# Performance work log

Measured on AMD Instinct MI355X. Metric: run time of the kernel, lower is better.

Reference implementation:

```python
import jax, jax.numpy as jnp
import numpy as np

N = 65536      # total nodes (cells) in batch
E = 262144     # edges per edge type
T = 3          # edge types: row, col, diag
D = 128        # hidden_dim
HG = 4         # gat_heads
DHG = D // HG  # 32, GAT head dim
HH = 4         # hgt_heads
DHH = D // HH  # 32, HGT head dim
B = 32         # boards per batch
SLOPE = 0.2
EPS = 1e-6


def setup_inputs():
    ks = jax.random.split(jax.random.key(0), 32)
    def nrm(i, shape, s=0.05):
        return (jax.random.normal(ks[i], shape) * s).astype(jnp.float32)
    inp = {
        'x_cell': nrm(0, (N, D), 1.0),
        'z_h': nrm(1, (B, D), 1.0),
        'x_cell_embedded': nrm(2, (N, D), 1.0),
        'edge_index': jax.random.randint(ks[3], (T, 2, E), 0, N, dtype=jnp.int32),
        'batch_size': B,
        # GAT conv 1 (one GATConv per edge type, summed)
        'gat1_W': nrm(4, (T, D, D), 0.09),
        'gat1_asrc': nrm(5, (T, HG, DHG), 0.12),
        'gat1_adst': nrm(6, (T, HG, DHG), 0.12),
        'gat1_b': jnp.zeros((T, D), jnp.float32),
        # GAT conv 2
        'gat2_W': nrm(7, (T, D, D), 0.09),
        'gat2_asrc': nrm(8, (T, HG, DHG), 0.12),
        'gat2_adst': nrm(9, (T, HG, DHG), 0.12),
        'gat2_b': jnp.zeros((T, D), jnp.float32),
        # RMSNorms
        'norm1_s': jnp.ones((D,), jnp.float32),
        'norm2_s': jnp.ones((D,), jnp.float32),
        'norm3_s': jnp.ones((D,), jnp.float32),
        # HGT (single node type 'cell', T edge types)
        'hgt_Wk': nrm(10, (D, D), 0.09), 'hgt_bk': jnp.zeros((D,), jnp.float32),
        'hgt_Wq': nrm(11, (D, D), 0.09), 'hgt_bq': jnp.zeros((D,), jnp.float32),
        'hgt_Wv': nrm(12, (D, D), 0.09), 'hgt_bv': jnp.zeros((D,), jnp.float32),
        'hgt_arel': nrm(13, (T, HH, DHH, DHH), 0.15),
        'hgt_mrel': nrm(14, (T, HH, DHH, DHH), 0.15),
        'hgt_prel': jnp.ones((T, HH), jnp.float32),
        'hgt_Wo': nrm(15, (D, D), 0.09), 'hgt_bo': jnp.zeros((D,), jnp.float32),
        'hgt_skip': jnp.ones((), jnp.float32),
        # input injection
        'inj_W': nrm(16, (D, D), 0.09), 'inj_b': jnp.zeros((D,), jnp.float32),
        # FiLM
        'film_W1': nrm(17, (D, 2 * D), 0.09), 'film_b1': jnp.zeros((2 * D,), jnp.float32),
        'film_W2': nrm(18, (2 * D, 2 * D), 0.001), 'film_b2': jnp.zeros((2 * D,), jnp.float32),
    }
    return inp


def _rmsnorm(x, scale):
    return scale * x * jax.lax.rsqrt(jnp.mean(x * x, axis=-1, keepdims=True) + EPS)


def _res(x_old, x_new, scale):
    return jax.nn.leaky_relu(x_old + _rmsnorm(x_new, scale), SLOPE)


def _gat_sum(x, W, asrc, adst, b, src, dst):
    """HeteroConv(sum) over T GATConvs (concat heads, add_self_loops)."""
    loop = jnp.arange(N, dtype=src.dtype)
    def one(Wt, a_s, a_d, bt, s, t):
        s = jnp.concatenate([s, loop])   # self loops
        t = jnp.concatenate([t, loop])
        h = (x @ Wt).reshape(N, HG, DHG)             # [N,H,Dh]
        alpha_src = (h * a_s).sum(-1)                # [N,H]
        alpha_dst = (h * a_d).sum(-1)
        e = jax.nn.leaky_relu(alpha_src[s] + alpha_dst[t], SLOPE)  # [E+N,H]
        m = jax.ops.segment_max(e, t, num_segments=N)
        ex = jnp.exp(e - m[t])
        denom = jax.ops.segment_sum(ex, t, num_segments=N)
        alpha = ex / (denom[t] + 1e-16)
        out = jax.ops.segment_sum(alpha[:, :, None] * h[s], t, num_segments=N)
        return out.reshape(N, D) + bt
    return jax.vmap(one)(W, asrc, adst, b, src, dst).sum(0)


def _hgt(x, Wk, bk, Wq, bq, Wv, bv, a_rel, m_rel, p_rel, Wo, bo, skip, src, dst):
    k = (x @ Wk + bk).reshape(N, HH, DHH)
    q = (x @ Wq + bq).reshape(N, HH, DHH)
    v = (x @ Wv + bv).reshape(N, HH, DHH)
    # per-edge-type relation transforms at node level, then gather per edge
    k_t = jnp.einsum('nhd,thdf->tnhf', k, a_rel)    # [T,N,H,Dk]
    v_t = jnp.einsum('nhd,thdf->tnhf', v, m_rel)
    k_e = jax.vmap(lambda a, i: a[i])(k_t, src)     # [T,E,H,Dk]
    v_e = jax.vmap(lambda a, i: a[i])(v_t, src)
    score = (q[dst] * k_e).sum(-1) * p_rel[:, None, :] / np.sqrt(DHH)  # [T,E,H]
    score = score.reshape(T * E, HH)
    dst_f = dst.reshape(-1)
    m = jax.ops.segment_max(score, dst_f, num_segments=N)
    ex = jnp.exp(score - m[dst_f])
    denom = jax.ops.segment_sum(ex, dst_f, num_segments=N)
    alpha = ex / (denom[dst_f] + 1e-16)
    agg = jax.ops.segment_sum(alpha[:, :, None] * v_e.reshape(T * E, HH, DHH),
                              dst_f, num_segments=N)          # [N,H,Dk]
    out = jax.nn.gelu(agg.reshape(N, D), approximate=False) @ Wo + bo
    sig = jax.nn.sigmoid(skip)
    return sig * out + (1.0 - sig) * x


def _film(nodes, z_h, W1, b1, W2, b2, bsz):
    gb = jax.nn.gelu(z_h @ W1 + b1, approximate=False) @ W2 + b2  # [B,2D]
    gamma, beta = jnp.split(gb, 2, axis=-1)
    gamma = 0.1 * jnp.tanh(gamma)
    beta = 0.1 * jnp.tanh(beta)
    c = N // bsz
    out = (1.0 + gamma)[:, None, :] * nodes.reshape(bsz, c, D) + beta[:, None, :]
    return out.reshape(N, D)


def reference(x_cell, z_h, x_cell_embedded,
              gat1_W, gat1_asrc, gat1_adst, gat1_b,
              gat2_W, gat2_asrc, gat2_adst, gat2_b,
              norm1_s, norm2_s, norm3_s,
              hgt_Wk, hgt_bk, hgt_Wq, hgt_bq, hgt_Wv, hgt_bv,
              hgt_arel, hgt_mrel, hgt_prel, hgt_Wo, hgt_bo, hgt_skip,
              inj_W, inj_b, film_W1, film_b1, film_W2, film_b2,
              edge_index, batch_size):
    src = edge_index[:, 0]
    dst = edge_index[:, 1]
    x1 = _res(x_cell, _gat_sum(x_cell, gat1_W, gat1_asrc, gat1_adst, gat1_b, src, dst), norm1_s)
    x2 = _res(x1, _gat_sum(x1, gat2_W, gat2_asrc, gat2_adst, gat2_b, src, dst), norm2_s)
    x3 = _res(x2, _hgt(x2, hgt_Wk, hgt_bk, hgt_Wq, hgt_bq, hgt_Wv, hgt_bv,
                       hgt_arel, hgt_mrel, hgt_prel, hgt_Wo, hgt_bo, hgt_skip,
                       src, dst), norm3_s)
    x3 = x3 + x_cell_embedded @ inj_W + inj_b
    return _film(x3, z_h, film_W1, film_b1, film_W2, film_b2, batch_size)
```

## Files before the change

kernel.cpp:

```cpp
#include <hip/hip_runtime.h>

#define NN 65536
#define EE 262144
#define ND ((size_t)NN * 128)
#define TBW 132
#define WLP 136

typedef unsigned short u16;
typedef short bf8_t __attribute__((ext_vector_type(8)));
typedef float f32x4 __attribute__((ext_vector_type(4)));

__device__ __forceinline__ float lrelu(float x){ return x > 0.f ? x : 0.2f*x; }
__device__ __forceinline__ float gelu_exact(float x){ return 0.5f*x*(1.f+erff(x*0.70710678118654752f)); }
__device__ __forceinline__ u16 f2bf(float f){
    union { float f; unsigned u; } v; v.f = f;
    unsigned u = v.u;
    return (u16)((u + 0x7FFFu + ((u >> 16) & 1u)) >> 16);
}
__device__ __forceinline__ float bf2f(u16 b){
    union { unsigned u; float f; } v; v.u = ((unsigned)b) << 16; return v.f;
}
__device__ __forceinline__ float2 bf2x(unsigned p){
    union { unsigned u; float f; } a, b;
    a.u = (p & 0xFFFFu) << 16; b.u = p & 0xFFFF0000u;
    return make_float2(a.f, b.f);
}
__device__ __forceinline__ unsigned cvt2(float a, float b){
    unsigned r; asm("v_cvt_pk_bf16_f32 %0, %1, %2" : "=v"(r) : "v"(a), "v"(b)); return r;
}

__device__ __forceinline__ void load_af32(const float* __restrict__ X, int row, int lk, bf8_t* af){
    #pragma unroll
    for (int kk = 0; kk < 4; ++kk){
        const float* p = X + (size_t)row*128 + kk*32 + lk*8;
        float4 a = *(const float4*)p;
        float4 b = *(const float4*)(p+4);
        union { bf8_t v; unsigned u[4]; } r;
        r.u[0] = cvt2(a.x, a.y); r.u[1] = cvt2(a.z, a.w);
        r.u[2] = cvt2(b.x, b.y); r.u[3] = cvt2(b.z, b.w);
        af[kk] = r.v;
    }
}
__device__ __forceinline__ void load_af16(const u16* __restrict__ X, int row, int lk, bf8_t* af){
    #pragma unroll
    for (int kk = 0; kk < 4; ++kk)
        af[kk] = *(const bf8_t*)(X + (size_t)row*128 + kk*32 + lk*8);
}

__device__ __forceinline__ void stage_w(const u16* __restrict__ src, u16* __restrict__ wl, int tid){
    #pragma unroll
    for (int j = 0; j < 8; ++j){
        int o = (j*256 + tid)*8;
        bf8_t v = *(const bf8_t*)(src + o);
        *(bf8_t*)(wl + ((o>>7)*WLP + (o&127))) = v;
    }
}

__device__ __forceinline__ void mfma_l1_acc(const bf8_t* af, const u16* __restrict__ wl,
                                            int lr, int lk, f32x4* acc){
    #pragma unroll
    for (int kk = 0; kk < 4; ++kk){
        bf8_t B[8];
        #pragma unroll
        for (int nt = 0; nt < 8; ++nt)
            B[nt] = *(const bf8_t*)&wl[(nt*16+lr)*WLP + kk*32 + lk*8];
        #pragma unroll
        for (int nt = 0; nt < 8; ++nt)
            acc[nt] = __builtin_amdgcn_mfma_f32_16x16x32_bf16(af[kk], B[nt], acc[nt], 0, 0, 0);
    }
}
__device__ __forceinline__ void mfma_l1(const bf8_t* af, const u16* __restrict__ wl,
                                        int lr, int lk, f32x4* acc){
    #pragma unroll
    for (int i = 0; i < 8; ++i) acc[i] = (f32x4){0.f,0.f,0.f,0.f};
    mfma_l1_acc(af, wl, lr, lk, acc);
}
__device__ __forceinline__ void mfma_l2(const bf8_t* af0, const bf8_t* af1,
                                        const u16* __restrict__ wl,
                                        int lr, int lk, f32x4* acc0, f32x4* acc1){
    #pragma unroll
    for (int i = 0; i < 8; ++i){ acc0[i] = (f32x4){0.f,0.f,0.f,0.f}; acc1[i] = (f32x4){0.f,0.f,0.f,0.f}; }
    #pragma unroll
    for (int kk = 0; kk < 4; ++kk){
        bf8_t B[8];
        #pragma unroll
        for (int nt = 0; nt < 8; ++nt)
            B[nt] = *(const bf8_t*)&wl[(nt*16+lr)*WLP + kk*32 + lk*8];
        #pragma unroll
        for (int nt = 0; nt < 8; ++nt){
            acc0[nt] = __builtin_amdgcn_mfma_f32_16x16x32_bf16(af0[kk], B[nt], acc0[nt], 0, 0, 0);
            acc1[nt] = __builtin_amdgcn_mfma_f32_16x16x32_bf16(af1[kk], B[nt], acc1[nt], 0, 0, 0);
        }
    }
}

__device__ __forceinline__ void acc_to_tb(u16 (*tbw)[TBW], const f32x4* acc, int lr, int lk, const float* bias){
    asm volatile("s_waitcnt lgkmcnt(0)" ::: "memory");
    #pragma unroll
    for (int nt = 0; nt < 8; ++nt){
        int col = nt*16 + lr;
        float badd = bias ? bias[col] : 0.f;
        #pragma unroll
        for (int i = 0; i < 4; ++i) tbw[lk*4+i][col] = f2bf(acc[nt][i] + badd);
    }
    asm volatile("s_waitcnt lgkmcnt(0)" ::: "memory");
}
__device__ __forceinline__ void acc_to_tb_gelu(u16 (*tbw)[TBW], const f32x4* acc, int lr, int lk){
    asm volatile("s_waitcnt lgkmcnt(0)" ::: "memory");
    #pragma unroll
    for (int nt = 0; nt < 8; ++nt){
        int col = nt*16 + lr;
        #pragma unroll
        for (int i = 0; i < 4; ++i) tbw[lk*4+i][col] = f2bf(gelu_exact(acc[nt][i]));
    }
    asm volatile("s_waitcnt lgkmcnt(0)" ::: "memory");
}
__device__ __forceinline__ void tb_store(const u16 (*tbw)[TBW], u16* __restrict__ O, size_t rowstride, int rowbase, int lr, int lk){
    #pragma unroll
    for (int c = 0; c < 4; ++c){
        bf8_t v = *(const bf8_t*)&tbw[c*4+lk][lr*8];
        *(bf8_t*)(O + (size_t)(rowbase + c*4 + lk)*rowstride + lr*8) = v;
    }
}
__device__ __forceinline__ void tb_frags(const u16 (*tbw)[TBW], int lr, int lk, bf8_t* ha){
    #pragma unroll
    for (int kk = 0; kk < 4; ++kk) ha[kk] = *(const bf8_t*)&tbw[lr][kk*32 + lk*8];
}
__device__ __forceinline__ void tb_rows(const u16 (*tbw)[TBW], int lr, int lk, bf8_t* rw){
    #pragma unroll
    for (int c = 0; c < 4; ++c) rw[c] = *(const bf8_t*)&tbw[c*4+lk][lr*8];
}

__global__ __launch_bounds__(256) void wpack_k(
    const float* __restrict__ g1W, const float* __restrict__ g2W,
    const float* __restrict__ Wk, const float* __restrict__ Wq, const float* __restrict__ Wv,
    const float* __restrict__ Wo, const float* __restrict__ injW,
    const float* __restrict__ arel, const float* __restrict__ mrel,
    const float* __restrict__ g1as, const float* __restrict__ g1ad,
    const float* __restrict__ g2as, const float* __restrict__ g2ad,
    u16* __restrict__ wp, u16* __restrict__ wpa)
{
    int b = blockIdx.x, tid = threadIdx.x;
    if (b < 17) {
        const float* src; int rel = 0;
        if (b < 3) src = g1W + b*16384;
        else if (b < 6) src = g2W + (b-3)*16384;
        else if (b == 6) src = Wk;
        else if (b == 7) src = Wq;
        else if (b == 8) src = Wv;
        else if (b == 9) src = Wo;
        else if (b == 10) src = injW;
        else if (b < 14) { src = arel + (b-11)*4096; rel = 2; }
        else { src = mrel + (b-14)*4096; rel = 1; }
        u16* dst = wp + (size_t)b*16384;
        for (int idx = tid; idx < 16384; idx += 256) {
            int n = idx >> 7, k = idx & 127;
            float v;
            if (rel == 1)      v = ((n>>5)==(k>>5)) ? src[(n>>5)*1024 + (k&31)*32 + (n&31)] : 0.f;
            else if (rel == 2) v = ((n>>5)==(k>>5)) ? src[(n>>5)*1024 + (n&31)*32 + (k&31)] : 0.f;
            else               v = src[k*128 + n];
            dst[idx] = f2bf(v);
        }
    } else {
        for (int idx = tid; idx < 6*2048; idx += 256) {
            int m = idx >> 11;
            int j = idx & 2047;
            int cg = j >> 7, k = j & 127;
            const float* as = (m < 3) ? g1as : g2as;
            const float* ad = (m < 3) ? g1ad : g2ad;
            int t = (m < 3) ? m : m - 3;
            float v = 0.f;
            if (cg < 4)      { if ((k>>5)==cg)   v = as[t*128 + cg*32 + (k&31)]; }
            else if (cg < 8) { int g = cg-4; if ((k>>5)==g) v = ad[t*128 + g*32 + (k&31)]; }
            wpa[idx] = f2bf(v);
        }
    }
}

template<int AF32>
__global__ __launch_bounds__(256, 3) void gat_gemm3_k(const float* __restrict__ Xf, const u16* __restrict__ Xb,
    const u16* __restrict__ wpg, const u16* __restrict__ wpa,
    u16* __restrict__ hb, float* __restrict__ alsb, float* __restrict__ aldb)
{
    __shared__ __align__(16) u16 wl[128*WLP];
    __shared__ __align__(16) u16 tb[4][16][TBW];
    const int tid = threadIdx.x, wave = tid>>6, lane = tid&63, lr = lane&15, lk = lane>>4;
    const int t = blockIdx.y;
    const int rw0 = blockIdx.x*128 + wave*32;
    bf8_t af0[4], af1[4];
    if (AF32){ load_af32(Xf, rw0 + lr, lk, af0); load_af32(Xf, rw0 + 16 + lr, lk, af1); }
    else     { load_af16(Xb, rw0 + lr, lk, af0); load_af16(Xb, rw0 + 16 + lr, lk, af1); }
    stage_w(wpg + t*16384, wl, tid);
    bf8_t Ba[4];
    #pragma unroll
    for (int kk = 0; kk < 4; ++kk)
        Ba[kk] = *(const bf8_t*)&wpa[t*2048 + lr*128 + kk*32 + lk*8];
    __syncthreads();
    f32x4 acc0[8], acc1[8];
    mfma_l2(af0, af1, wl, lr, lk, acc0, acc1);
    u16* h = hb + (size_t)t*ND;
    float* alst = alsb + (size_t)t*NN*4;
    float* aldt = aldb + (size_t)t*NN*4;
    {
        acc_to_tb(tb[wave], acc0, lr, lk, nullptr);
        tb_store(tb[wave], h, 128, rw0, lr, lk);
        bf8_t ha[4]; tb_frags(tb[wave], lr, lk, ha);
        f32x4 a2 = (f32x4){0.f,0.f,0.f,0.f};
        #pragma unroll
        for (int kk = 0; kk < 4; ++kk)
            a2 = __builtin_amdgcn_mfma_f32_16x16x32_bf16(ha[kk], Ba[kk], a2, 0, 0, 0);
        if (lr < 8){
            float* dp = (lr < 4) ? alst : aldt;
            int g = lr & 3;
            #pragma unroll
            for (int i = 0; i < 4; ++i) dp[(size_t)(rw0 + lk*4 + i)*4 + g] = a2[i];
        }
    }
    {
        acc_to_tb(tb[wave], acc1, lr, lk, nullptr);
        tb_store(tb[wave], h, 128, rw0 + 16, lr, lk);
        bf8_t ha[4]; tb_frags(tb[wave], lr, lk, ha);
        f32x4 a2 = (f32x4){0.f,0.f,0.f,0.f};
        #pragma unroll
        for (int kk = 0; kk < 4; ++kk)
            a2 = __builtin_amdgcn_mfma_f32_16x16x32_bf16(ha[kk], Ba[kk], a2, 0, 0, 0);
        if (lr < 8){
            float* dp = (lr < 4) ? alst : aldt;
            int g = lr & 3;
            #pragma unroll
            for (int i = 0; i < 4; ++i) dp[(size_t)(rw0 + 16 + lk*4 + i)*4 + g] = a2[i];
        }
    }
}

__global__ __launch_bounds__(256, 3) void hgt_proj_k(const u16* __restrict__ X,
    const u16* __restrict__ wpk, const u16* __restrict__ wpq, const u16* __restrict__ wpv,
    const u16* __restrict__ wparel,
    const float* __restrict__ bk, const float* __restrict__ bq, const float* __restrict__ bv,
    u16* __restrict__ kvb, u16* __restrict__ qtb)
{
    __shared__ __align__(16) u16 wl[128*WLP];
    __shared__ __align__(16) u16 tb[4][16][TBW];
    const int tid = threadIdx.x, wave = tid>>6, lane = tid&63, lr = lane&15, lk = lane>>4;
    const int task = blockIdx.y;
    const int rw0 = blockIdx.x*128 + wave*32;
    bf8_t af0[4], af1[4];
    load_af16(X, rw0 + lr, lk, af0);
    load_af16(X, rw0 + 16 + lr, lk, af1);
    f32x4 acc0[8], acc1[8];
    if (task == 0) {
        stage_w(wpk, wl, tid);
        __syncthreads();
        mfma_l2(af0, af1, wl, lr, lk, acc0, acc1);
        acc_to_tb(tb[wave], acc0, lr, lk, bk); tb_store(tb[wave], kvb, 256, rw0, lr, lk);
        acc_to_tb(tb[wave], acc1, lr, lk, bk); tb_store(tb[wave], kvb, 256, rw0 + 16, lr, lk);
    } else if (task == 1) {
        stage_w(wpv, wl, tid);
        __syncthreads();
        mfma_l2(af0, af1, wl, lr, lk, acc0, acc1);
        acc_to_tb(tb[wave], acc0, lr, lk, bv); tb_store(tb[wave], kvb + 128, 256, rw0, lr, lk);
        acc_to_tb(tb[wave], acc1, lr, lk, bv); tb_store(tb[wave], kvb + 128, 256, rw0 + 16, lr, lk);
    } else {
        const int t = task - 2;
        stage_w(wpq, wl, tid);
        __syncthreads();
        mfma_l2(af0, af1, wl, lr, lk, acc0, acc1);
        bf8_t ha0[4], ha1[4];
        acc_to_tb(tb[wave], acc0, lr, lk, bq); tb_frags(tb[wave], lr, lk, ha0);
        acc_to_tb(tb[wave], acc1, lr, lk, bq); tb_frags(tb[wave], lr, lk, ha1);
        __syncthreads();
        stage_w(wparel + t*16384, wl, tid);
        __syncthreads();
        mfma_l2(ha0, ha1, wl, lr, lk, acc0, acc1);
        u16* o = qtb + (size_t)t*ND;
        acc_to_tb(tb[wave], acc0, lr, lk, nullptr); tb_store(tb[wave], o, 128, rw0, lr, lk);
        acc_to_tb(tb[wave], acc1, lr, lk, nullptr); tb_store(tb[wave], o, 128, rw0 + 16, lr, lk);
    }
}

__global__ __launch_bounds__(256) void hgt_agg_k(const u16* __restrict__ kvb,
    const u16* __restrict__ qtb, const float* __restrict__ prel,
    const int* __restrict__ moff, const int* __restrict__ msrc,
    u16* __restrict__ pb)
{
    int gid = blockIdx.x*256 + threadIdx.x;
    int node = gid >> 6, lane = gid & 63;
    int hh = lane >> 4;
    const float S = 0.17677669529663689f;
    float2 qv0 = bf2x(*(const unsigned*)&qtb[(size_t)node*128 + lane*2]);
    float2 qv1 = bf2x(*(const unsigned*)&qtb[ND + (size_t)node*128 + lane*2]);
    float2 qv2 = bf2x(*(const unsigned*)&qtb[2*ND + (size_t)node*128 + lane*2]);
    float ph0 = prel[hh]*S, ph1 = prel[4+hh]*S, ph2 = prel[8+hh]*S;
    float dsum = 0.f;
    float a00=0.f,a01=0.f,a10=0.f,a11=0.f,a20=0.f,a21=0.f;
    int beg = moff[node], end = moff[node+1];
    int e = beg;
    for (; e + 8 <= end; e += 8) {
        int sp[8]; unsigned kw[8], vw[8];
        #pragma unroll
        for (int j = 0; j < 8; ++j) sp[j] = msrc[e+j];
        #pragma unroll
        for (int j = 0; j < 8; ++j){
            size_t ro = (size_t)(sp[j] & 0xFFFF)*256 + lane*2;
            kw[j] = *(const unsigned*)&kvb[ro];
            vw[j] = *(const unsigned*)&kvb[ro + 128];
        }
        #pragma unroll
        for (int j = 0; j < 8; ++j){
            int tt = sp[j] >> 16;
            float qx = tt==0 ? qv0.x : (tt==1 ? qv1.x : qv2.x);
            float qy = tt==0 ? qv0.y : (tt==1 ? qv1.y : qv2.y);
            float2 k2 = bf2x(kw[j]);
            float sc = qx*k2.x + qy*k2.y;
            #pragma unroll
            for (int o = 1; o < 16; o <<= 1) sc += __shfl_xor(sc, o);
            float ph = tt==0 ? ph0 : (tt==1 ? ph1 : ph2);
            float ex = expf(sc * ph);
            float2 v2 = bf2x(vw[j]);
            float e0 = tt==0?ex:0.f, e1 = tt==1?ex:0.f, e2 = tt==2?ex:0.f;
            dsum += ex;
            a00 += e0*v2.x; a01 += e0*v2.y;
            a10 += e1*v2.x; a11 += e1*v2.y;
            a20 += e2*v2.x; a21 += e2*v2.y;
        }
    }
    for (; e < end; ++e) {
        int sp = msrc[e];
        int tt = sp >> 16;
        size_t ro = (size_t)(sp & 0xFFFF)*256 + lane*2;
        float2 k2 = bf2x(*(const unsigned*)&kvb[ro]);
        float qx = tt==0 ? qv0.x : (tt==1 ? qv1.x : qv2.x);
        float qy = tt==0 ? qv0.y : (tt==1 ? qv1.y : qv2.y);
        float sc = qx*k2.x + qy*k2.y;
        #pragma unroll
        for (int o = 1; o < 16; o <<= 1) sc += __shfl_xor(sc, o);
        float ph = tt==0 ? ph0 : (tt==1 ? ph1 : ph2);
        float ex = expf(sc * ph);
        float2 v2 = bf2x(*(const unsigned*)&kvb[ro + 128]);
        float e0 = tt==0?ex:0.f, e1 = tt==1?ex:0.f, e2 = tt==2?ex:0.f;
        dsum += ex;
        a00 += e0*v2.x; a01 += e0*v2.y;
        a10 += e1*v2.x; a11 += e1*v2.y;
        a20 += e2*v2.x; a21 += e2*v2.y;
    }
    float inv = 1.f/(dsum + 1e-16f);
    size_t o = (size_t)node*128 + lane*2;
    *(unsigned*)&pb[o]        = cvt2(a00*inv, a01*inv);
    *(unsigned*)&pb[ND + o]   = cvt2(a10*inv, a11*inv);
    *(unsigned*)&pb[2*ND + o] = cvt2(a20*inv, a21*inv);
}

__global__ __launch_bounds__(256, 3) void final_k(const u16* __restrict__ pb,
    const u16* __restrict__ wpmrel, const u16* __restrict__ wpo, const float* __restrict__ bo,
    const u16* __restrict__ x2b, const float* __restrict__ skipp, const float* __restrict__ scale,
    const float* __restrict__ xemb, const u16* __restrict__ wpinj, const float* __restrict__ injb,
    const float* __restrict__ gbuf, const int* __restrict__ bszp,
    float* __restrict__ out)
{
    __shared__ __align__(16) u16 wl[128*WLP];
    __shared__ __align__(16) u16 tb[4][16][TBW];
    const int tid = threadIdx.x, wave = tid>>6, lane = tid&63, lr = lane&15, lk = lane>>4;
    const int rw = blockIdx.x*64 + wave*16;
    f32x4 acc[8];
    #pragma unroll
    for (int i = 0; i < 8; ++i) acc[i] = (f32x4){0.f,0.f,0.f,0.f};
    for (int t = 0; t < 3; ++t){
        if (t) __syncthreads();
        bf8_t a0[4]; load_af16(pb + (size_t)t*ND, rw + lr, lk, a0);
        stage_w(wpmrel + t*16384, wl, tid);
        __syncthreads();
        mfma_l1_acc(a0, wl, lr, lk, acc);
    }
    bf8_t ga[4];
    acc_to_tb_gelu(tb[wave], acc, lr, lk);
    tb_frags(tb[wave], lr, lk, ga);
    __syncthreads();
    stage_w(wpo, wl, tid);
    __syncthreads();
    mfma_l1(ga, wl, lr, lk, acc);
    bf8_t hw[4];
    acc_to_tb(tb[wave], acc, lr, lk, bo);
    tb_rows(tb[wave], lr, lk, hw);
    bf8_t e0[4];
    load_af32(xemb, rw + lr, lk, e0);
    __syncthreads();
    stage_w(wpinj, wl, tid);
    __syncthreads();
    mfma_l1(e0, wl, lr, lk, acc);
    bf8_t in[4];
    acc_to_tb(tb[wave], acc, lr, lk, injb);
    tb_rows(tb[wave], lr, lk, in);
    const float sig = 1.f/(1.f + expf(-skipp[0]));
    const int cpb = NN / *bszp;
    float4 sca = *(const float4*)&scale[lr*8];
    float4 scb = *(const float4*)&scale[lr*8 + 4];
    #pragma unroll
    for (int c = 0; c < 4; ++c){
        int row = rw + c*4 + lk;
        bf8_t x8 = *(const bf8_t*)(x2b + (size_t)row*128 + lr*8);
        float x[8], v[8];
        float ssl = 0.f;
        #pragma unroll
        for (int j = 0; j < 8; ++j){
            x[j] = bf2f((u16)x8[j]);
            float h = bf2f((u16)hw[c][j]);
            v[j] = sig*h + (1.f - sig)*x[j];
            ssl += v[j]*v[j];
        }
        ssl += __shfl_xor(ssl, 1); ssl += __shfl_xor(ssl, 2);
        ssl += __shfl_xor(ssl, 4); ssl += __shfl_xor(ssl, 8);
        float rq = rsqrtf(ssl*(1.f/128.f) + 1e-6f);
        const float* gr = gbuf + (row / cpb)*256;
        float4 g0 = *(const float4*)&gr[lr*8];
        float4 g1 = *(const float4*)&gr[lr*8 + 4];
        float4 b0 = *(const float4*)&gr[128 + lr*8];
        float4 b1 = *(const float4*)&gr[128 + lr*8 + 4];
        float4 oA, oB;
        #pragma unroll
        for (int j = 0; j < 8; ++j){
            float scj = (j < 4) ? ((const float*)&sca)[j] : ((const float*)&scb)[j-4];
            float y = lrelu(x[j] + scj*v[j]*rq);
            float hf = y + bf2f((u16)in[c][j]);
            float gj = (j < 4) ? ((const float*)&g0)[j] : ((const float*)&g1)[j-4];
            float bj = (j < 4) ? ((const float*)&b0)[j] : ((const float*)&b1)[j-4];
            float ov = (1.f + gj)*hf + bj;
            if (j < 4) ((float*)&oA)[j] = ov; else ((float*)&oB)[j-4] = ov;
        }
        *(float4*)(out + (size_t)row*128 + lr*8)     = oA;
        *(float4*)(out + (size_t)row*128 + lr*8 + 4) = oB;
    }
}

__global__ __launch_bounds__(256) void hist_k(const int* __restrict__ ei, int* __restrict__ cnt){
    int gid = blockIdx.x*256 + threadIdx.x;
    int t = gid / EE, e = gid - t*EE;
    int d = ei[t*2*EE + EE + e];
    atomicAdd(&cnt[d], 1);
}
__global__ __launch_bounds__(256) void scan1_k(const int* __restrict__ cnt, int* __restrict__ off, int* __restrict__ parts){
    __shared__ int sums[256];
    int b = blockIdx.x; int base = b * 1024;
    int tid = threadIdx.x;
    int v[4]; int tsum = 0;
    int gbase = base + tid*4;
    #pragma unroll
    for (int i = 0; i < 4; ++i){ v[i] = cnt[gbase+i]; tsum += v[i]; }
    sums[tid] = tsum; __syncthreads();
    for (int ofs = 1; ofs < 256; ofs <<= 1) {
        int a = (tid >= ofs) ? sums[tid-ofs] : 0;
        __syncthreads();
        sums[tid] += a;
        __syncthreads();
    }
    int run = sums[tid] - tsum;
    int obase = base + tid*4;
    #pragma unroll
    for (int i = 0; i < 4; ++i){ off[obase+i] = run; run += v[i]; }
    if (tid == 255) parts[b] = sums[255];
}
__global__ void scan2_k(int* parts){
    if (threadIdx.x == 0 && blockIdx.x == 0) {
        int run = 0;
        for (int i = 0; i < 64; ++i) { int v = parts[i]; parts[i] = run; run += v; }
    }
}
__global__ __launch_bounds__(256) void scan3_k(int* __restrict__ off, const int* __restrict__ parts){
    int b = blockIdx.x; int base = b * 1024;
    int add = parts[b];
    int idx = base + threadIdx.x*4;
    #pragma unroll
    for (int i = 0; i < 4; ++i) off[idx+i] += add;
    if (b == 0 && threadIdx.x == 0) off[NN] = 3*EE;
}
__global__ __launch_bounds__(256) void scatter_k(const int* __restrict__ ei, const int* __restrict__ off,
                                                 int* __restrict__ cur, int* __restrict__ out){
    int gid = blockIdx.x*256 + threadIdx.x;
    int t = gid / EE, e = gid - t*EE;
    int s = ei[t*2*EE + e];
    int d = ei[t*2*EE + EE + e];
    int p = atomicAdd(&cur[d], 1);
    out[off[d] + p] = s | (t << 16);
}

template<int XF32>
__global__ __launch_bounds__(256) void gat_aggres_k(const u16* __restrict__ hb,
    const float* __restrict__ alsb, const float* __restrict__ aldb,
    const int* __restrict__ moff, const int* __restrict__ msrc,
    const float* __restrict__ bias3, const float* __restrict__ xoldf, const u16* __restrict__ xoldb,
    const float* __restrict__ scale, u16* __restrict__ outb)
{
    int gid = blockIdx.x*256 + threadIdx.x;
    int node = gid >> 6, lane = gid & 63;
    int g = lane >> 4;
    float ad0 = aldb[(size_t)node*4 + g];
    float ad1 = aldb[((size_t)NN + node)*4 + g];
    float ad2 = aldb[((size_t)2*NN + node)*4 + g];
    float dsum0, dsum1, dsum2, s00, s01, s10, s11, s20, s21;
    {
        float ex = expf(lrelu(alsb[(size_t)node*4 + g] + ad0));
        float2 hv = bf2x(*(const unsigned*)&hb[(size_t)node*128 + lane*2]);
        dsum0 = ex; s00 = ex*hv.x; s01 = ex*hv.y;
    }
    {
        float ex = expf(lrelu(alsb[((size_t)NN + node)*4 + g] + ad1));
        float2 hv = bf2x(*(const unsigned*)&hb[((size_t)NN + node)*128 + lane*2]);
        dsum1 = ex; s10 = ex*hv.x; s11 = ex*hv.y;
    }
    {
        float ex = expf(lrelu(alsb[((size_t)2*NN + node)*4 + g] + ad2));
        float2 hv = bf2x(*(const unsigned*)&hb[((size_t)2*NN + node)*128 + lane*2]);
        dsum2 = ex; s20 = ex*hv.x; s21 = ex*hv.y;
    }
    int beg = moff[node], end = moff[node+1];
    int e = beg;
    for (; e + 8 <= end; e += 8) {
        int sp[8]; unsigned hp[8]; float av[8];
        #pragma unroll
        for (int j = 0; j < 8; ++j) sp[j] = msrc[e+j];
        #pragma unroll
        for (int j = 0; j < 8; ++j){
            hp[j] = *(const unsigned*)&hb[(size_t)sp[j]*128 + lane*2];
            av[j] = alsb[(size_t)sp[j]*4 + g];
        }
        #pragma unroll
        for (int j = 0; j < 8; ++j){
            int tt = sp[j] >> 16;
            float adt = tt==0 ? ad0 : (tt==1 ? ad1 : ad2);
            float ex = expf(lrelu(av[j] + adt));
            float2 w = bf2x(hp[j]);
            float e0 = tt==0?ex:0.f, e1 = tt==1?ex:0.f, e2 = tt==2?ex:0.f;
            dsum0 += e0; dsum1 += e1; dsum2 += e2;
            s00 += e0*w.x; s01 += e0*w.y;
            s10 += e1*w.x; s11 += e1*w.y;
            s20 += e2*w.x; s21 += e2*w.y;
        }
    }
    for (; e < end; ++e) {
        int sp = msrc[e];
        int tt = sp >> 16;
        unsigned hp = *(const unsigned*)&hb[(size_t)sp*128 + lane*2];
        float av = alsb[(size_t)sp*4 + g];
        float adt = tt==0 ? ad0 : (tt==1 ? ad1 : ad2);
        float ex = expf(lrelu(av + adt));
        float2 w = bf2x(hp);
        float e0 = tt==0?ex:0.f, e1 = tt==1?ex:0.f, e2 = tt==2?ex:0.f;
        dsum0 += e0; dsum1 += e1; dsum2 += e2;
        s00 += e0*w.x; s01 += e0*w.y;
        s10 += e1*w.x; s11 += e1*w.y;
        s20 += e2*w.x; s21 += e2*w.y;
    }
    float a0 = s00/(dsum0+1e-16f) + s10/(dsum1+1e-16f) + s20/(dsum2+1e-16f);
    float a1 = s01/(dsum0+1e-16f) + s11/(dsum1+1e-16f) + s21/(dsum2+1e-16f);
    int c0 = lane*2;
    a0 += bias3[c0]   + bias3[128+c0]   + bias3[256+c0];
    a1 += bias3[c0+1] + bias3[128+c0+1] + bias3[256+c0+1];
    float ssum = a0*a0 + a1*a1;
    #pragma unroll
    for (int o = 1; o < 64; o <<= 1) ssum += __shfl_xor(ssum, o);
    float r = rsqrtf(ssum*(1.f/128.f) + 1e-6f);
    size_t off = (size_t)node*128 + c0;
    float2 xo;
    if (XF32) xo = *(const float2*)&xoldf[off];
    else      xo = bf2x(*(const unsigned*)&xoldb[off]);
    float y0 = lrelu(xo.x + scale[c0]*a0*r);
    float y1 = lrelu(xo.y + scale[c0+1]*a1*r);
    *(unsigned*)&outb[off] = cvt2(y0, y1);
}

__global__ __launch_bounds__(256) void film_k(const float* __restrict__ z,
    const float* __restrict__ W1, const float* __restrict__ b1,
    const float* __restrict__ W2, const float* __restrict__ b2,
    float* __restrict__ gb)
{
    __shared__ float zr[128];
    __shared__ float g1[256];
    int r = blockIdx.x, tid = threadIdx.x;
    if (tid < 128) zr[tid] = z[r*128 + tid];
    __syncthreads();
    float s = b1[tid];
    for (int k = 0; k < 128; ++k) s += zr[k]*W1[k*256 + tid];
    g1[tid] = gelu_exact(s);
    __syncthreads();
    float s2 = b2[tid];
    for (int k = 0; k < 256; ++k) s2 += g1[k]*W2[k*256 + tid];
    gb[r*256 + tid] = 0.1f*tanhf(s2);
}

extern "C" void kernel_launch(void* const* d_in, const int* in_sizes, int n_in,
                              void* d_out, int out_size, void* d_ws, size_t ws_size,
                              hipStream_t stream)
{
    const float* x_cell = (const float*)d_in[0];
    const float* z_h    = (const float*)d_in[1];
    const float* x_emb  = (const float*)d_in[2];
    const int*   eidx   = (const int*)d_in[3];
    const int*   bszp   = (const int*)d_in[4];
    const float* g1W  = (const float*)d_in[5];
    const float* g1as = (const float*)d_in[6];
    const float* g1ad = (const float*)d_in[7];
    const float* g1b  = (const float*)d_in[8];
    const float* g2W  = (const float*)d_in[9];
    const float* g2as = (const float*)d_in[10];
    const float* g2ad = (const float*)d_in[11];
    const float* g2b  = (const float*)d_in[12];
    const float* n1s  = (const float*)d_in[13];
    const float* n2s  = (const float*)d_in[14];
    const float* n3s  = (const float*)d_in[15];
    const float* Wk   = (const float*)d_in[16];
    const float* bk   = (const float*)d_in[17];
    const float* Wq   = (const float*)d_in[18];
    const float* bq   = (const float*)d_in[19];
    const float* Wv   = (const float*)d_in[20];
    const float* bv   = (const float*)d_in[21];
    const float* arel = (const float*)d_in[22];
    const float* mrel = (const float*)d_in[23];
    const float* prel = (const float*)d_in[24];
    const float* Wo   = (const float*)d_in[25];
    const float* bo   = (const float*)d_in[26];
    const float* skipp= (const float*)d_in[27];
    const float* injW = (const float*)d_in[28];
    const float* injb = (const float*)d_in[29];
    const float* fW1  = (const float*)d_in[30];
    const float* fb1  = (const float*)d_in[31];
    const float* fW2  = (const float*)d_in[32];
    const float* fb2  = (const float*)d_in[33];

    u16* wp   = (u16*)d_ws;
    u16* wpa  = wp + (size_t)17*16384;
    u16* x1b  = wpa + 6*2048;
    u16* x2b  = x1b + ND;
    u16* kvb  = x2b + ND;
    u16* pb   = kvb + 2*ND;
    u16* hb   = pb + 3*ND;
    float* alsb = (float*)(hb + 3*ND);
    float* aldb = alsb + (size_t)3*NN*4;
    float* gbuf = aldb + (size_t)3*NN*4;
    int* coff   = (int*)(gbuf + 32*256);
    int* csrc   = coff + 3*(NN+1);
    int* tmpc   = csrc + 3*EE;
    int* parts  = tmpc + 3*NN;

    u16* qtb = hb;
    float* outp = (float*)d_out;

    const u16* wpg1 = wp;
    const u16* wpg2 = wp + (size_t)3*16384;
    const u16* wpk  = wp + (size_t)6*16384;
    const u16* wpq  = wp + (size_t)7*16384;
    const u16* wpv  = wp + (size_t)8*16384;
    const u16* wpo  = wp + (size_t)9*16384;
    const u16* wpinj= wp + (size_t)10*16384;
    const u16* wparel = wp + (size_t)11*16384;
    const u16* wpmrel = wp + (size_t)14*16384;

    wpack_k<<<18, 256, 0, stream>>>(g1W, g2W, Wk, Wq, Wv, Wo, injW, arel, mrel,
                                    g1as, g1ad, g2as, g2ad, wp, wpa);

    hipMemsetAsync(tmpc, 0, NN*sizeof(int), stream);
    hist_k<<<3*EE/256, 256, 0, stream>>>(eidx, tmpc);
    scan1_k<<<64, 256, 0, stream>>>(tmpc, coff, parts);
    scan2_k<<<1, 64, 0, stream>>>(parts);
    scan3_k<<<64, 256, 0, stream>>>(coff, parts);
    hipMemsetAsync(tmpc, 0, NN*sizeof(int), stream);
    scatter_k<<<3*EE/256, 256, 0, stream>>>(eidx, coff, tmpc, csrc);

    int B = in_sizes[1] / 128;
    film_k<<<B, 256, 0, stream>>>(z_h, fW1, fb1, fW2, fb2, gbuf);

    gat_gemm3_k<1><<<dim3(512,3), 256, 0, stream>>>(x_cell, nullptr, wpg1, wpa, hb, alsb, aldb);
    gat_aggres_k<1><<<16384, 256, 0, stream>>>(hb, alsb, aldb, coff, csrc, g1b, x_cell, nullptr, n1s, x1b);

    gat_gemm3_k<0><<<dim3(512,3), 256, 0, stream>>>(nullptr, x1b, wpg2, wpa + 3*2048, hb, alsb, aldb);
    gat_aggres_k<0><<<16384, 256, 0, stream>>>(hb, alsb, aldb, coff, csrc, g2b, nullptr, x1b, n2s, x2b);

    hgt_proj_k<<<dim3(512,5), 256, 0, stream>>>(x2b, wpk, wpq, wpv, wparel,
                                                bk, bq, bv, kvb, qtb);
    hgt_agg_k<<<16384, 256, 0, stream>>>(kvb, qtb, prel, coff, csrc, pb);

    final_k<<<1024, 256, 0, stream>>>(pb, wpmrel, wpo, bo, x2b, skipp, n3s,
                                      x_emb, wpinj, injb, gbuf, bszp, outp);
}
```

Baseline: 620.6 us.

## Segment CSR by edge type with self-loops and precompute GAT edge alphas

The CSR is rebuilt so each destination node has three contiguous per-type segments, each starting with an explicit self-loop slot. A scatter-time position map records where each edge lands. A new alpha_k kernel computes exp(leaky_relu) attention weights once per edge, stored in CSR order. The GAT and HGT aggregation kernels then loop per type without per-edge type selects or redundant per-lane exp work, and read attention weights contiguously. The cost is extra preprocessing kernels, a larger CSR, and a ~15 MB alpha buffer written and read per GAT layer. Shorter per-type inner loops with 4-wide unrolling may also expose less memory-level parallelism.

Result: no change. 609.2 us (-1.8%).

```diff
diff --git a/kernel.cpp b/kernel.cpp
--- a/kernel.cpp
+++ b/kernel.cpp
@@ -5,6 +5,8 @@
 #define ND ((size_t)NN * 128)
 #define TBW 132
 #define WLP 136
+#define NTOT (EE + NN)
+#define CSRN (3*EE + 3*NN)
 
 typedef unsigned short u16;
 typedef short bf8_t __attribute__((ext_vector_type(8)));
@@ -278,76 +280,223 @@
     }
 }
 
+__global__ __launch_bounds__(256) void hist_k(const int* __restrict__ ei, int* __restrict__ cnt){
+    int gid = blockIdx.x*256 + threadIdx.x;
+    int t = gid / EE, e = gid - t*EE;
+    int d = ei[t*2*EE + EE + e];
+    atomicAdd(&cnt[t*NN + d], 1);
+}
+__global__ __launch_bounds__(256) void scanA_k(const int* __restrict__ cnt, int* __restrict__ s0off, int* __restrict__ parts){
+    __shared__ int sums[256];
+    int b = blockIdx.x; int base = b * 1024;
+    int tid = threadIdx.x;
+    int v[4]; int tsum = 0;
+    #pragma unroll
+    for (int i = 0; i < 4; ++i){
+        int n = base + tid*4 + i;
+        v[i] = cnt[n] + cnt[NN+n] + cnt[2*NN+n] + 3;
+        tsum += v[i];
+    }
+    sums[tid] = tsum; __syncthreads();
+    for (int ofs = 1; ofs < 256; ofs <<= 1) {
+        int a = (tid >= ofs) ? sums[tid-ofs] : 0;
+        __syncthreads();
+        sums[tid] += a;
+        __syncthreads();
+    }
+    int run = sums[tid] - tsum;
+    #pragma unroll
+    for (int i = 0; i < 4; ++i){ s0off[base + tid*4 + i] = run; run += v[i]; }
+    if (tid == 255) parts[b] = sums[255];
+}
+__global__ void scan2_k(int* parts){
+    if (threadIdx.x == 0 && blockIdx.x == 0) {
+        int run = 0;
+        for (int i = 0; i < 64; ++i) { int v = parts[i]; parts[i] = run; run += v; }
+    }
+}
+__global__ __launch_bounds__(256) void scanB_k(const int* __restrict__ cnt, int* __restrict__ s0off,
+                                               int* __restrict__ s1off, int* __restrict__ s2off,
+                                               const int* __restrict__ parts){
+    int b = blockIdx.x; int base = b * 1024;
+    int add = parts[b];
+    #pragma unroll
+    for (int i = 0; i < 4; ++i){
+        int n = base + threadIdx.x*4 + i;
+        int m = s0off[n] + add;
+        int c0 = cnt[n], c1 = cnt[NN+n];
+        s0off[n] = m;
+        s1off[n] = m + c0 + 1;
+        s2off[n] = m + c0 + c1 + 2;
+    }
+    if (b == 0 && threadIdx.x == 0) s0off[NN] = CSRN;
+}
+__global__ __launch_bounds__(256) void selffill_k(const int* __restrict__ s0off, const int* __restrict__ s1off,
+                                                  const int* __restrict__ s2off, int* __restrict__ csrc){
+    int gid = blockIdx.x*256 + threadIdx.x;
+    int t = gid / NN, n = gid - t*NN;
+    int pos = (t==0) ? s0off[n] : (t==1 ? s1off[n] : s2off[n]);
+    csrc[pos] = n;
+}
+__global__ __launch_bounds__(256) void scatter_k(const int* __restrict__ ei,
+    const int* __restrict__ s0off, const int* __restrict__ s1off, const int* __restrict__ s2off,
+    int* __restrict__ cur, int* __restrict__ csrc, int* __restrict__ posmap){
+    int gid = blockIdx.x*256 + threadIdx.x;
+    int t = gid / EE, e = gid - t*EE;
+    int s = ei[t*2*EE + e];
+    int d = ei[t*2*EE + EE + e];
+    int p = atomicAdd(&cur[t*NN + d], 1);
+    int basep = (t==0) ? s0off[d] : (t==1 ? s1off[d] : s2off[d]);
+    int pos = basep + 1 + p;
+    csrc[pos] = s;
+    posmap[t*EE + e] = pos;
+}
+
+__global__ __launch_bounds__(256) void alpha_k(const float* __restrict__ alsb, const float* __restrict__ aldb,
+    const int* __restrict__ ei, const int* __restrict__ posmap,
+    const int* __restrict__ s0off, const int* __restrict__ s1off, const int* __restrict__ s2off,
+    float4* __restrict__ ab)
+{
+    int gid = blockIdx.x*256 + threadIdx.x;
+    int t = gid / NTOT, r = gid - t*NTOT;
+    int s, d, pos;
+    if (r < EE) {
+        s = ei[t*2*EE + r];
+        d = ei[t*2*EE + EE + r];
+        pos = posmap[t*EE + r];
+    } else {
+        int n = r - EE;
+        s = n; d = n;
+        pos = (t==0) ? s0off[n] : (t==1 ? s1off[n] : s2off[n]);
+    }
+    const float* As = alsb + ((size_t)t*NN + s)*4;
+    const float* Ad = aldb + ((size_t)t*NN + d)*4;
+    float4 o;
+    o.x = expf(lrelu(As[0] + Ad[0]));
+    o.y = expf(lrelu(As[1] + Ad[1]));
+    o.z = expf(lrelu(As[2] + Ad[2]));
+    o.w = expf(lrelu(As[3] + Ad[3]));
+    ab[pos] = o;
+}
+
+template<int XF32>
+__global__ __launch_bounds__(256) void gat_aggres_k(const u16* __restrict__ hb,
+    const float* __restrict__ abf,
+    const int* __restrict__ s0off, const int* __restrict__ s1off, const int* __restrict__ s2off,
+    const int* __restrict__ csrc,
+    const float* __restrict__ bias3, const float* __restrict__ xoldf, const u16* __restrict__ xoldb,
+    const float* __restrict__ scale, u16* __restrict__ outb)
+{
+    int gid = blockIdx.x*256 + threadIdx.x;
+    int node = gid >> 6, lane = gid & 63;
+    int g = lane >> 4;
+    int segb[4] = { s0off[node], s1off[node], s2off[node], s0off[node+1] };
+    float a0 = 0.f, a1 = 0.f;
+    for (int t = 0; t < 3; ++t) {
+        const u16* h = hb + (size_t)t*ND;
+        int beg = segb[t], end = segb[t+1];
+        float s0 = 0.f, s1 = 0.f, ds = 0.f;
+        int pos = beg;
+        for (; pos + 4 <= end; pos += 4) {
+            int sA = csrc[pos], sB = csrc[pos+1], sC = csrc[pos+2], sD = csrc[pos+3];
+            float alA = abf[(size_t)pos*4 + g];
+            float alB = abf[(size_t)(pos+1)*4 + g];
+            float alC = abf[(size_t)(pos+2)*4 + g];
+            float alD = abf[(size_t)(pos+3)*4 + g];
+            unsigned hA = *(const unsigned*)&h[(size_t)sA*128 + lane*2];
+            unsigned hB = *(const unsigned*)&h[(size_t)sB*128 + lane*2];
+            unsigned hC = *(const unsigned*)&h[(size_t)sC*128 + lane*2];
+            unsigned hD = *(const unsigned*)&h[(size_t)sD*128 + lane*2];
+            float2 wA = bf2x(hA), wB = bf2x(hB), wC = bf2x(hC), wD = bf2x(hD);
+            ds += alA + alB + alC + alD;
+            s0 += alA*wA.x + alB*wB.x + alC*wC.x + alD*wD.x;
+            s1 += alA*wA.y + alB*wB.y + alC*wC.y + alD*wD.y;
+        }
+        for (; pos < end; ++pos) {
+            int s = csrc[pos];
+            float al = abf[(size_t)pos*4 + g];
+            unsigned hp = *(const unsigned*)&h[(size_t)s*128 + lane*2];
+            float2 w = bf2x(hp);
+            ds += al; s0 += al*w.x; s1 += al*w.y;
+        }
+        float inv = 1.f/(ds + 1e-16f);
+        a0 += s0*inv; a1 += s1*inv;
+    }
+    int c0 = lane*2;
+    a0 += bias3[c0]   + bias3[128+c0]   + bias3[256+c0];
+    a1 += bias3[c0+1] + bias3[128+c0+1] + bias3[256+c0+1];
+    float ssum = a0*a0 + a1*a1;
+    #pragma unroll
+    for (int o = 1; o < 64; o <<= 1) ssum += __shfl_xor(ssum, o);
+    float r = rsqrtf(ssum*(1.f/128.f) + 1e-6f);
+    size_t off = (size_t)node*128 + c0;
+    float2 xo;
+    if (XF32) xo = *(const float2*)&xoldf[off];
+    else      xo = bf2x(*(const unsigned*)&xoldb[off]);
+    float y0 = lrelu(xo.x + scale[c0]*a0*r);
+    float y1 = lrelu(xo.y + scale[c0+1]*a1*r);
+    *(unsigned*)&outb[off] = cvt2(y0, y1);
+}
+
 __global__ __launch_bounds__(256) void hgt_agg_k(const u16* __restrict__ kvb,
     const u16* __restrict__ qtb, const float* __restrict__ prel,
-    const int* __restrict__ moff, const int* __restrict__ msrc,
-    u16* __restrict__ pb)
+    const int* __restrict__ s0off, const int* __restrict__ s1off, const int* __restrict__ s2off,
+    const int* __restrict__ csrc, u16* __restrict__ pb)
 {
     int gid = blockIdx.x*256 + threadIdx.x;
     int node = gid >> 6, lane = gid & 63;
     int hh = lane >> 4;
     const float S = 0.17677669529663689f;
-    float2 qv0 = bf2x(*(const unsigned*)&qtb[(size_t)node*128 + lane*2]);
-    float2 qv1 = bf2x(*(const unsigned*)&qtb[ND + (size_t)node*128 + lane*2]);
-    float2 qv2 = bf2x(*(const unsigned*)&qtb[2*ND + (size_t)node*128 + lane*2]);
-    float ph0 = prel[hh]*S, ph1 = prel[4+hh]*S, ph2 = prel[8+hh]*S;
+    int segb[4] = { s0off[node], s1off[node], s2off[node], s0off[node+1] };
     float dsum = 0.f;
-    float a00=0.f,a01=0.f,a10=0.f,a11=0.f,a20=0.f,a21=0.f;
-    int beg = moff[node], end = moff[node+1];
-    int e = beg;
-    for (; e + 8 <= end; e += 8) {
-        int sp[8]; unsigned kw[8], vw[8];
-        #pragma unroll
-        for (int j = 0; j < 8; ++j) sp[j] = msrc[e+j];
-        #pragma unroll
-        for (int j = 0; j < 8; ++j){
-            size_t ro = (size_t)(sp[j] & 0xFFFF)*256 + lane*2;
-            kw[j] = *(const unsigned*)&kvb[ro];
-            vw[j] = *(const unsigned*)&kvb[ro + 128];
-        }
-        #pragma unroll
-        for (int j = 0; j < 8; ++j){
-            int tt = sp[j] >> 16;
-            float qx = tt==0 ? qv0.x : (tt==1 ? qv1.x : qv2.x);
-            float qy = tt==0 ? qv0.y : (tt==1 ? qv1.y : qv2.y);
-            float2 k2 = bf2x(kw[j]);
-            float sc = qx*k2.x + qy*k2.y;
+    float a0[3], a1[3];
+    for (int t = 0; t < 3; ++t) {
+        a0[t] = 0.f; a1[t] = 0.f;
+        float ph = prel[t*4 + hh] * S;
+        float2 qv = bf2x(*(const unsigned*)&qtb[(size_t)t*ND + (size_t)node*128 + lane*2]);
+        int beg = segb[t] + 1, end = segb[t+1];
+        int pos = beg;
+        for (; pos + 4 <= end; pos += 4) {
+            int sA = csrc[pos], sB = csrc[pos+1], sC = csrc[pos+2], sD = csrc[pos+3];
+            size_t rA = (size_t)sA*256 + lane*2, rB = (size_t)sB*256 + lane*2;
+            size_t rC = (size_t)sC*256 + lane*2, rD = (size_t)sD*256 + lane*2;
+            unsigned kA = *(const unsigned*)&kvb[rA], kB = *(const unsigned*)&kvb[rB];
+            unsigned kC = *(const unsigned*)&kvb[rC], kD = *(const unsigned*)&kvb[rD];
+            unsigned vA = *(const unsigned*)&kvb[rA+128], vB = *(const unsigned*)&kvb[rB+128];
+            unsigned vC = *(const unsigned*)&kvb[rC+128], vD = *(const unsigned*)&kvb[rD+128];
+            float2 k2A = bf2x(kA), k2B = bf2x(kB), k2C = bf2x(kC), k2D = bf2x(kD);
+            float scA = qv.x*k2A.x + qv.y*k2A.y;
+            float scB = qv.x*k2B.x + qv.y*k2B.y;
+            float scC = qv.x*k2C.x + qv.y*k2C.y;
+            float scD = qv.x*k2D.x + qv.y*k2D.y;
+            #pragma unroll
+            for (int o = 1; o < 16; o <<= 1){
+                scA += __shfl_xor(scA, o); scB += __shfl_xor(scB, o);
+                scC += __shfl_xor(scC, o); scD += __shfl_xor(scD, o);
+            }
+            float eA = expf(scA*ph), eB = expf(scB*ph), eC = expf(scC*ph), eD = expf(scD*ph);
+            float2 v2A = bf2x(vA), v2B = bf2x(vB), v2C = bf2x(vC), v2D = bf2x(vD);
+            dsum += eA + eB + eC + eD;
+            a0[t] += eA*v2A.x + eB*v2B.x + eC*v2C.x + eD*v2D.x;
+            a1[t] += eA*v2A.y + eB*v2B.y + eC*v2C.y + eD*v2D.y;
+        }
+        for (; pos < end; ++pos) {
+            int s = csrc[pos];
+            size_t ro = (size_t)s*256 + lane*2;
+            float2 k2 = bf2x(*(const unsigned*)&kvb[ro]);
+            float sc = qv.x*k2.x + qv.y*k2.y;
             #pragma unroll
             for (int o = 1; o < 16; o <<= 1) sc += __shfl_xor(sc, o);
-            float ph = tt==0 ? ph0 : (tt==1 ? ph1 : ph2);
             float ex = expf(sc * ph);
-            float2 v2 = bf2x(vw[j]);
-            float e0 = tt==0?ex:0.f, e1 = tt==1?ex:0.f, e2 = tt==2?ex:0.f;
-            dsum += ex;
-            a00 += e0*v2.x; a01 += e0*v2.y;
-            a10 += e1*v2.x; a11 += e1*v2.y;
-            a20 += e2*v2.x; a21 += e2*v2.y;
-        }
-    }
-    for (; e < end; ++e) {
-        int sp = msrc[e];
-        int tt = sp >> 16;
-        size_t ro = (size_t)(sp & 0xFFFF)*256 + lane*2;
-        float2 k2 = bf2x(*(const unsigned*)&kvb[ro]);
-        float qx = tt==0 ? qv0.x : (tt==1 ? qv1.x : qv2.x);
-        float qy = tt==0 ? qv0.y : (tt==1 ? qv1.y : qv2.y);
-        float sc = qx*k2.x + qy*k2.y;
-        #pragma unroll
-        for (int o = 1; o < 16; o <<= 1) sc += __shfl_xor(sc, o);
-        float ph = tt==0 ? ph0 : (tt==1 ? ph1 : ph2);
-        float ex = expf(sc * ph);
-        float2 v2 = bf2x(*(const unsigned*)&kvb[ro + 128]);
-        float e0 = tt==0?ex:0.f, e1 = tt==1?ex:0.f, e2 = tt==2?ex:0.f;
-        dsum += ex;
-        a00 += e0*v2.x; a01 += e0*v2.y;
-        a10 += e1*v2.x; a11 += e1*v2.y;
-        a20 += e2*v2.x; a21 += e2*v2.y;
+            float2 v2 = bf2x(*(const unsigned*)&kvb[ro + 128]);
+            dsum += ex; a0[t] += ex*v2.x; a1[t] += ex*v2.y;
+        }
     }
     float inv = 1.f/(dsum + 1e-16f);
     size_t o = (size_t)node*128 + lane*2;
-    *(unsigned*)&pb[o]        = cvt2(a00*inv, a01*inv);
-    *(unsigned*)&pb[ND + o]   = cvt2(a10*inv, a11*inv);
-    *(unsigned*)&pb[2*ND + o] = cvt2(a20*inv, a21*inv);
+    *(unsigned*)&pb[o]        = cvt2(a0[0]*inv, a1[0]*inv);
+    *(unsigned*)&pb[ND + o]   = cvt2(a0[1]*inv, a1[1]*inv);
+    *(unsigned*)&pb[2*ND + o] = cvt2(a0[2]*inv, a1[2]*inv);
 }
 
 __global__ __launch_bounds__(256, 3) void final_k(const u16* __restrict__ pb,
@@ -429,142 +578,6 @@
         *(float4*)(out + (size_t)row*128 + lr*8)     = oA;
         *(float4*)(out + (size_t)row*128 + lr*8 + 4) = oB;
     }
-}
-
-__global__ __launch_bounds__(256) void hist_k(const int* __restrict__ ei, int* __restrict__ cnt){
-    int gid = blockIdx.x*256 + threadIdx.x;
-    int t = gid / EE, e = gid - t*EE;
-    int d = ei[t*2*EE + EE + e];
-    atomicAdd(&cnt[d], 1);
-}
-__global__ __launch_bounds__(256) void scan1_k(const int* __restrict__ cnt, int* __restrict__ off, int* __restrict__ parts){
-    __shared__ int sums[256];
-    int b = blockIdx.x; int base = b * 1024;
-    int tid = threadIdx.x;
-    int v[4]; int tsum = 0;
-    int gbase = base + tid*4;
-    #pragma unroll
-    for (int i = 0; i < 4; ++i){ v[i] = cnt[gbase+i]; tsum += v[i]; }
-    sums[tid] = tsum; __syncthreads();
-    for (int ofs = 1; ofs < 256; ofs <<= 1) {
-        int a = (tid >= ofs) ? sums[tid-ofs] : 0;
-        __syncthreads();
-        sums[tid] += a;
-        __syncthreads();
-    }
-    int run = sums[tid] - tsum;
-    int obase = base + tid*4;
-    #pragma unroll
-    for (int i = 0; i < 4; ++i){ off[obase+i] = run; run += v[i]; }
-    if (tid == 255) parts[b] = sums[255];
-}
-__global__ void scan2_k(int* parts){
-    if (threadIdx.x == 0 && blockIdx.x == 0) {
-        int run = 0;
-        for (int i = 0; i < 64; ++i) { int v = parts[i]; parts[i] = run; run += v; }
-    }
-}
-__global__ __launch_bounds__(256) void scan3_k(int* __restrict__ off, const int* __restrict__ parts){
-    int b = blockIdx.x; int base = b * 1024;
-    int add = parts[b];
-    int idx = base + threadIdx.x*4;
-    #pragma unroll
-    for (int i = 0; i < 4; ++i) off[idx+i] += add;
-    if (b == 0 && threadIdx.x == 0) off[NN] = 3*EE;
-}
-__global__ __launch_bounds__(256) void scatter_k(const int* __restrict__ ei, const int* __restrict__ off,
-                                                 int* __restrict__ cur, int* __restrict__ out){
-    int gid = blockIdx.x*256 + threadIdx.x;
-    int t = gid / EE, e = gid - t*EE;
-    int s = ei[t*2*EE + e];
-    int d = ei[t*2*EE + EE + e];
-    int p = atomicAdd(&cur[d], 1);
-    out[off[d] + p] = s | (t << 16);
-}
-
-template<int XF32>
-__global__ __launch_bounds__(256) void gat_aggres_k(const u16* __restrict__ hb,
-    const float* __restrict__ alsb, const float* __restrict__ aldb,
-    const int* __restrict__ moff, const int* __restrict__ msrc,
-    const float* __restrict__ bias3, const float* __restrict__ xoldf, const u16* __restrict__ xoldb,
-    const float* __restrict__ scale, u16* __restrict__ outb)
-{
-    int gid = blockIdx.x*256 + threadIdx.x;
-    int node = gid >> 6, lane = gid & 63;
-    int g = lane >> 4;
-    float ad0 = aldb[(size_t)node*4 + g];
-    float ad1 = aldb[((size_t)NN + node)*4 + g];
-    float ad2 = aldb[((size_t)2*NN + node)*4 + g];
-    float dsum0, dsum1, dsum2, s00, s01, s10, s11, s20, s21;
-    {
-        float ex = expf(lrelu(alsb[(size_t)node*4 + g] + ad0));
-        float2 hv = bf2x(*(const unsigned*)&hb[(size_t)node*128 + lane*2]);
-        dsum0 = ex; s00 = ex*hv.x; s01 = ex*hv.y;
-    }
-    {
-        float ex = expf(lrelu(alsb[((size_t)NN + node)*4 + g] + ad1));
-        float2 hv = bf2x(*(const unsigned*)&hb[((size_t)NN + node)*128 + lane*2]);
-        dsum1 = ex; s10 = ex*hv.x; s11 = ex*hv.y;
-    }
-    {
-        float ex = expf(lrelu(alsb[((size_t)2*NN + node)*4 + g] + ad2));
-        float2 hv = bf2x(*(const unsigned*)&hb[((size_t)2*NN + node)*128 + lane*2]);
-        dsum2 = ex; s20 = ex*hv.x; s21 = ex*hv.y;
-    }
-    int beg = moff[node], end = moff[node+1];
-    int e = beg;
-    for (; e + 8 <= end; e += 8) {
-        int sp[8]; unsigned hp[8]; float av[8];
-        #pragma unroll
-        for (int j = 0; j < 8; ++j) sp[j] = msrc[e+j];
-        #pragma unroll
-        for (int j = 0; j < 8; ++j){
-            hp[j] = *(const unsigned*)&hb[(size_t)sp[j]*128 + lane*2];
-            av[j] = alsb[(size_t)sp[j]*4 + g];
-        }
-        #pragma unroll
-        for (int j = 0; j < 8; ++j){
-            int tt = sp[j] >> 16;
-            float adt = tt==0 ? ad0 : (tt==1 ? ad1 : ad2);
-            float ex = expf(lrelu(av[j] + adt));
-            float2 w = bf2x(hp[j]);
-            float e0 = tt==0?ex:0.f, e1 = tt==1?ex:0.f, e2 = tt==2?ex:0.f;
-            dsum0 += e0; dsum1 += e1; dsum2 += e2;
-            s00 += e0*w.x; s01 += e0*w.y;
-            s10 += e1*w.x; s11 += e1*w.y;
-            s20 += e2*w.x; s21 += e2*w.y;
-        }
-    }
-    for (; e < end; ++e) {
-        int sp = msrc[e];
-        int tt = sp >> 16;
-        unsigned hp = *(const unsigned*)&hb[(size_t)sp*128 + lane*2];
-        float av = alsb[(size_t)sp*4 + g];
-        float adt = tt==0 ? ad0 : (tt==1 ? ad1 : ad2);
-        float ex = expf(lrelu(av + adt));
-        float2 w = bf2x(hp);
-        float e0 = tt==0?ex:0.f, e1 = tt==1?ex:0.f, e2 = tt==2?ex:0.f;
-        dsum0 += e0; dsum1 += e1; dsum2 += e2;
-        s00 += e0*w.x; s01 += e0*w.y;
-        s10 += e1*w.x; s11 += e1*w.y;
-        s20 += e2*w.x; s21 += e2*w.y;
-    }
-    float a0 = s00/(dsum0+1e-16f) + s10/(dsum1+1e-16f) + s20/(dsum2+1e-16f);
-    float a1 = s01/(dsum0+1e-16f) + s11/(dsum1+1e-16f) + s21/(dsum2+1e-16f);
-    int c0 = lane*2;
-    a0 += bias3[c0]   + bias3[128+c0]   + bias3[256+c0];
-    a1 += bias3[c0+1] + bias3[128+c0+1] + bias3[256+c0+1];
-    float ssum = a0*a0 + a1*a1;
-    #pragma unroll
-    for (int o = 1; o < 64; o <<= 1) ssum += __shfl_xor(ssum, o);
-    float r = rsqrtf(ssum*(1.f/128.f) + 1e-6f);
-    size_t off = (size_t)node*128 + c0;
-    float2 xo;
-    if (XF32) xo = *(const float2*)&xoldf[off];
-    else      xo = bf2x(*(const unsigned*)&xoldb[off]);
-    float y0 = lrelu(xo.x + scale[c0]*a0*r);
-    float y1 = lrelu(xo.y + scale[c0+1]*a1*r);
-    *(unsigned*)&outb[off] = cvt2(y0, y1);
 }
 
 __global__ __launch_bounds__(256) void film_k(const float* __restrict__ z,
@@ -627,7 +640,8 @@
 
     u16* wp   = (u16*)d_ws;
     u16* wpa  = wp + (size_t)17*16384;
-    u16* x1b  = wpa + 6*2048;
+    float4* ab = (float4*)(wpa + 6*2048);
+    u16* x1b  = (u16*)(ab + CSRN);
     u16* x2b  = x1b + ND;
     u16* kvb  = x2b + ND;
     u16* pb   = kvb + 2*ND;
@@ -635,10 +649,14 @@
     float* alsb = (float*)(hb + 3*ND);
     float* aldb = alsb + (size_t)3*NN*4;
     float* gbuf = aldb + (size_t)3*NN*4;
-    int* coff   = (int*)(gbuf + 32*256);
-    int* csrc   = coff + 3*(NN+1);
-    int* tmpc   = csrc + 3*EE;
-    int* parts  = tmpc + 3*NN;
+    int* s0off  = (int*)(gbuf + 32*256);
+    int* s1off  = s0off + (NN+1);
+    int* s2off  = s1off + NN;
+    int* csrc   = s2off + NN;
+    int* posmap = csrc + CSRN;
+    int* tmpc   = posmap + 3*EE;
+    int* cur    = tmpc + 3*NN;
+    int* parts  = cur + 3*NN;
 
     u16* qtb = hb;
     float* outp = (float*)d_out;
@@ -656,26 +674,31 @@
     wpack_k<<<18, 256, 0, stream>>>(g1W, g2W, Wk, Wq, Wv, Wo, injW, arel, mrel,
                                     g1as, g1ad, g2as, g2ad, wp, wpa);
 
-    hipMemsetAsync(tmpc, 0, NN*sizeof(int), stream);
+    hipMemsetAsync(tmpc, 0, 3*NN*sizeof(int), stream);
     hist_k<<<3*EE/256, 256, 0, stream>>>(eidx, tmpc);
-    scan1_k<<<64, 256, 0, stream>>>(tmpc, coff, parts);
+    scanA_k<<<64, 256, 0, stream>>>(tmpc, s0off, parts);
     scan2_k<<<1, 64, 0, stream>>>(parts);
-    scan3_k<<<64, 256, 0, stream>>>(coff, parts);
-    hipMemsetAsync(tmpc, 0, NN*sizeof(int), stream);
-    scatter_k<<<3*EE/256, 256, 0, stream>>>(eidx, coff, tmpc, csrc);
+    scanB_k<<<64, 256, 0, stream>>>(tmpc, s0off, s1off, s2off, parts);
+    selffill_k<<<3*NN/256, 256, 0, stream>>>(s0off, s1off, s2off, csrc);
+    hipMemsetAsync(cur, 0, 3*NN*sizeof(int), stream);
+    scatter_k<<<3*EE/256, 256, 0, stream>>>(eidx, s0off, s1off, s2off, cur, csrc, posmap);
 
     int B = in_sizes[1] / 128;
     film_k<<<B, 256, 0, stream>>>(z_h, fW1, fb1, fW2, fb2, gbuf);
 
     gat_gemm3_k<1><<<dim3(512,3), 256, 0, stream>>>(x_cell, nullptr, wpg1, wpa, hb, alsb, aldb);
-    gat_aggres_k<1><<<16384, 256, 0, stream>>>(hb, alsb, aldb, coff, csrc, g1b, x_cell, nullptr, n1s, x1b);
+    alpha_k<<<3*NTOT/256, 256, 0, stream>>>(alsb, aldb, eidx, posmap, s0off, s1off, s2off, ab);
+    gat_aggres_k<1><<<16384, 256, 0, stream>>>(hb, (const float*)ab, s0off, s1off, s2off, csrc,
+                                               g1b, x_cell, nullptr, n1s, x1b);
 
     gat_gemm3_k<0><<<dim3(512,3), 256, 0, stream>>>(nullptr, x1b, wpg2, wpa + 3*2048, hb, alsb, aldb);
-    gat_aggres_k<0><<<16384, 256, 0, stream>>>(hb, alsb, aldb, coff, csrc, g2b, nullptr, x1b, n2s, x2b);
+    alpha_k<<<3*NTOT/256, 256, 0, stream>>>(alsb, aldb, eidx, posmap, s0off, s1off, s2off, ab);
+    gat_aggres_k<0><<<16384, 256, 0, stream>>>(hb, (const float*)ab, s0off, s1off, s2off, csrc,
+                                               g2b, nullptr, x1b, n2s, x2b);
 
     hgt_proj_k<<<dim3(512,5), 256, 0, stream>>>(x2b, wpk, wpq, wpv, wparel,
                                                 bk, bq, bv, kvb, qtb);
-    hgt_agg_k<<<16384, 256, 0, stream>>>(kvb, qtb, prel, coff, csrc, pb);
+    hgt_agg_k<<<16384, 256, 0, stream>>>(kvb, qtb, prel, s0off, s1off, s2off, csrc, pb);
 
     final_k<<<1024, 256, 0, stream>>>(pb, wpmrel, wpo, bo, x2b, skipp, n3s,
                                       x_emb, wpinj, injb, gbuf, bszp, outp);
```
